# Optimization experiments

Hardware: AMD Instinct MI355X
Metric: run time of the kernel (lower is better)

## Reference

```python
import math
import jax, jax.numpy as jnp
import numpy as np

EMB = 768
HEADS = 12
HEAD_DIM = EMB // HEADS


def setup_inputs() -> dict:
    key = jax.random.key(0)
    k_x, k_wqkv, k_bqkv, k_wo, k_bo = jax.random.split(key, 5)
    B, N = 8, 1024
    lim_qkv = 1.0 / math.sqrt(EMB)
    lim_o = 1.0 / math.sqrt(EMB)
    return {
        "x": jax.random.normal(k_x, (B, N, EMB), dtype=jnp.float32),
        # torch nn.Linear convention: W has shape [out_features, in_features]
        "w_qkv": jax.random.uniform(k_wqkv, (3 * EMB, EMB), minval=-lim_qkv, maxval=lim_qkv, dtype=jnp.float32),
        "b_qkv": jax.random.uniform(k_bqkv, (3 * EMB,), minval=-lim_qkv, maxval=lim_qkv, dtype=jnp.float32),
        "w_out": jax.random.uniform(k_wo, (EMB, EMB), minval=-lim_o, maxval=lim_o, dtype=jnp.float32),
        "b_out": jax.random.uniform(k_bo, (EMB,), minval=-lim_o, maxval=lim_o, dtype=jnp.float32),
    }


def reference(x, w_qkv, b_qkv, w_out, b_out):
    B, N, _ = x.shape
    # fused QKV projection: [B, N, 3*EMB]
    qkv = jnp.einsum("bne,fe->bnf", x, w_qkv) + b_qkv
    qkv = qkv.reshape(B, N, 3, HEADS, HEAD_DIM)
    q, k, v = qkv[:, :, 0], qkv[:, :, 1], qkv[:, :, 2]  # [B, N, H, D]
    scale = 1.0 / math.sqrt(HEAD_DIM)
    # scores: [B, H, N, N]
    scores = jnp.einsum("bnhd,bmhd->bhnm", q, k) * scale
    attn = jax.nn.softmax(scores, axis=-1)
    # dropout is identity in eval mode (deterministic reference)
    out = jnp.einsum("bhnm,bmhd->bnhd", attn, v).reshape(B, N, EMB)
    out = jnp.einsum("bne,fe->bnf", out, w_out) + b_out
    return out, attn
```

## Files before the change

kernel.cpp:

```cpp
#include <hip/hip_runtime.h>
#include <hip/hip_bf16.h>
#include <cstddef>
#include <cstdint>

#define B_     8
#define N_     1024
#define EMB_   768
#define HEADS_ 12
#define HDIM_  64
#define M_TOK  (B_ * N_)
#define QKVF   (3 * EMB_)
#define OUT_ELEMS  ((size_t)M_TOK * EMB_)
#define ATTN_ELEMS ((size_t)B_ * HEADS_ * N_ * N_)

using short8  = __attribute__((ext_vector_type(8))) short;
using floatx4 = __attribute__((ext_vector_type(4))) float;

__device__ __forceinline__ short f32_to_bf16(float f) {
    union { float f; unsigned u; } x; x.f = f;
    unsigned r = x.u + 0x7FFFu + ((x.u >> 16) & 1u);
    return (short)(r >> 16);
}

__device__ __forceinline__ void gload_lds16(const void* g, void* l) {
    __builtin_amdgcn_global_load_lds(
        (const __attribute__((address_space(1))) void*)g,
        (__attribute__((address_space(3))) void*)l, 16, 0, 0);
}

__device__ __forceinline__ floatx4 mfma16(short8 a, short8 b, floatx4 c) {
    return __builtin_amdgcn_mfma_f32_16x16x32_bf16(a, b, c, 0, 0, 0);
}

__global__ __launch_bounds__(256) void cast_kernel(const float* __restrict__ in,
                                                   short* __restrict__ out) {
    const int i = (blockIdx.x * 256 + threadIdx.x) * 4;
    const float4 v = *reinterpret_cast<const float4*>(&in[i]);
    short s0 = f32_to_bf16(v.x), s1 = f32_to_bf16(v.y);
    short s2 = f32_to_bf16(v.z), s3 = f32_to_bf16(v.w);
    using short4v = __attribute__((ext_vector_type(4))) short;
    short4v s = {s0, s1, s2, s3};
    *reinterpret_cast<short4v*>(&out[i]) = s;
}

template <int OUT_BF16>
__global__ __launch_bounds__(256) void mfma_gemm_bt(
    const short* __restrict__ A, int lda,
    const short* __restrict__ Bm, int ldb,
    const float* __restrict__ bias,
    void* __restrict__ Cp, int ldc, int K)
{
    __shared__ short As[128 * 32];
    __shared__ short Bs[128 * 32];

    const int t = threadIdx.x, lane = t & 63, w = t >> 6;
    const int wy = w >> 1, wx = w & 1;
    const int row0 = blockIdx.y * 128;
    const int col0 = blockIdx.x * 128;
    const int m = lane & 15, kc = lane >> 4;
    const int sw = kc ^ ((m >> 1) & 3);

    floatx4 acc[4][4] = {};

    for (int k0 = 0; k0 < K; k0 += 32) {
        __syncthreads();
#pragma unroll
        for (int p = 0; p < 2; ++p) {
            const int ci = p * 256 + w * 64 + lane;
            const int r = ci >> 2, c = ci & 3;
            const int g = c ^ ((r >> 1) & 3);
            gload_lds16(&A[(size_t)(row0 + r) * lda + k0 + g * 8],
                        &As[(p * 256 + w * 64) * 8]);
            gload_lds16(&Bm[(size_t)(col0 + r) * ldb + k0 + g * 8],
                        &Bs[(p * 256 + w * 64) * 8]);
        }
        __syncthreads();

        short8 af[4], bf[4];
#pragma unroll
        for (int i = 0; i < 4; ++i)
            af[i] = *reinterpret_cast<const short8*>(
                &As[((wy * 64 + i * 16 + m) * 4 + sw) * 8]);
#pragma unroll
        for (int j = 0; j < 4; ++j)
            bf[j] = *reinterpret_cast<const short8*>(
                &Bs[((wx * 64 + j * 16 + m) * 4 + sw) * 8]);
#pragma unroll
        for (int i = 0; i < 4; ++i)
#pragma unroll
            for (int j = 0; j < 4; ++j)
                acc[i][j] = mfma16(af[i], bf[j], acc[i][j]);
    }

    const int rq = lane >> 4;
#pragma unroll
    for (int i = 0; i < 4; ++i) {
        const int rbase = row0 + wy * 64 + i * 16 + rq * 4;
#pragma unroll
        for (int j = 0; j < 4; ++j) {
            const int cc = col0 + wx * 64 + j * 16 + m;
            const float bb = bias[cc];
#pragma unroll
            for (int rg = 0; rg < 4; ++rg) {
                const float v = acc[i][j][rg] + bb;
                if (OUT_BF16)
                    ((short*)Cp)[(size_t)(rbase + rg) * ldc + cc] = f32_to_bf16(v);
                else
                    ((float*)Cp)[(size_t)(rbase + rg) * ldc + cc] = v;
            }
        }
    }
}

__global__ __launch_bounds__(256) void transpose_v(
    const short* __restrict__ qkv, short* __restrict__ Vt)
{
    __shared__ short T[64][72];
    const int bh = blockIdx.y, b = bh / HEADS_, h = bh % HEADS_;
    const int m0 = blockIdx.x * 64;
    const int t = threadIdx.x;
    const size_t vbase = (size_t)(b * N_) * QKVF + 2 * EMB_ + h * HDIM_;

#pragma unroll
    for (int p = 0; p < 2; ++p) {
        const int ci = p * 256 + t;
        const int r = ci >> 3, c = ci & 7;
        const short8 v = *reinterpret_cast<const short8*>(
            &qkv[vbase + (size_t)(m0 + r) * QKVF + c * 8]);
#pragma unroll
        for (int j = 0; j < 8; ++j) T[c * 8 + j][r] = v[j];
    }
    __syncthreads();
#pragma unroll
    for (int p = 0; p < 2; ++p) {
        const int ci = p * 256 + t;
        const int d = ci >> 3, c = ci & 7;
        short8 v;
#pragma unroll
        for (int j = 0; j < 8; ++j) v[j] = T[d][c * 8 + j];
        *reinterpret_cast<short8*>(&Vt[((size_t)bh * 64 + d) * N_ + m0 + c * 8]) = v;
    }
}

__global__ __launch_bounds__(256) void fused_attn(
    const short* __restrict__ qkv, const short* __restrict__ Vt,
    float* __restrict__ attn, short* __restrict__ O)
{
    __shared__ short Qs[128 * 64];
    __shared__ short Ks[2][64 * 64];
    __shared__ short Vs[2][64 * 64];
    __shared__ short Ps[128 * 72];
    __shared__ float rowM[128];
    __shared__ float rowS[128];

    const int t = threadIdx.x, lane = t & 63, w = t >> 6;
    const int bh = blockIdx.y, b = bh / HEADS_, h = bh % HEADS_;
    const int n0 = blockIdx.x * 128;
    const int m = lane & 15, kc = lane >> 4;
    const size_t qbase = (size_t)(b * N_) * QKVF + h * HDIM_;
    const size_t kbase = qbase + EMB_;

#define STAGE_K(buf, k0src)                                                   \
    do {                                                                      \
        _Pragma("unroll")                                                     \
        for (int p = 0; p < 2; ++p) {                                         \
            const int ci = p * 256 + w * 64 + lane;                           \
            const int r = ci >> 3, c = ci & 7;                                \
            const int g = c ^ (r & 7);                                        \
            gload_lds16(&qkv[kbase + (size_t)((k0src) + r) * QKVF + g * 8],   \
                        &Ks[buf][(p * 256 + w * 64) * 8]);                    \
        }                                                                     \
    } while (0)

#define STAGE_V(buf, k0src)                                                   \
    do {                                                                      \
        _Pragma("unroll")                                                     \
        for (int p = 0; p < 2; ++p) {                                         \
            const int ci = p * 256 + w * 64 + lane;                           \
            const int r = ci >> 3, c = ci & 7;                                \
            const int g = c ^ (r & 7);                                        \
            gload_lds16(&Vt[((size_t)bh * 64 + r) * N_ + (k0src) + g * 8],    \
                        &Vs[buf][(p * 256 + w * 64) * 8]);                    \
        }                                                                     \
    } while (0)

#pragma unroll
    for (int p = 0; p < 4; ++p) {
        const int ci = p * 256 + w * 64 + lane;
        const int r = ci >> 3, c = ci & 7;
        const int g = c ^ (r & 7);
        gload_lds16(&qkv[qbase + (size_t)(n0 + r) * QKVF + g * 8],
                    &Qs[(p * 256 + w * 64) * 8]);
    }
    STAGE_K(0, 0);
    __syncthreads();

    short8 qf[2][2];
#pragma unroll
    for (int i = 0; i < 2; ++i)
#pragma unroll
        for (int ks = 0; ks < 2; ++ks) {
            const int row = w * 32 + i * 16 + m;
            const int chunk = ks * 4 + kc;
            qf[i][ks] = *reinterpret_cast<const short8*>(
                &Qs[(row * 8 + (chunk ^ (m & 7))) * 8]);
        }

    float m_run[2][4], s_run[2][4];
#pragma unroll
    for (int i = 0; i < 2; ++i)
#pragma unroll
        for (int rg = 0; rg < 4; ++rg) { m_run[i][rg] = -1e30f; s_run[i][rg] = 0.0f; }

    for (int s = 0; s < 16; ++s) {
        const int cur = s & 1;
        if (s < 15) STAGE_K(cur ^ 1, (s + 1) * 64);

        floatx4 acc[2][4] = {};
#pragma unroll
        for (int ks = 0; ks < 2; ++ks) {
            const int chunk = ks * 4 + kc;
            const int pcs = chunk ^ (m & 7);
            short8 bfr[4];
#pragma unroll
            for (int j = 0; j < 4; ++j)
                bfr[j] = *reinterpret_cast<const short8*>(
                    &Ks[cur][((j * 16 + m) * 8 + pcs) * 8]);
#pragma unroll
            for (int i = 0; i < 2; ++i)
#pragma unroll
                for (int j = 0; j < 4; ++j)
                    acc[i][j] = mfma16(qf[i][ks], bfr[j], acc[i][j]);
        }

#pragma unroll
        for (int i = 0; i < 2; ++i)
#pragma unroll
            for (int rg = 0; rg < 4; ++rg) {
                const float x0 = acc[i][0][rg] * 0.125f;
                const float x1 = acc[i][1][rg] * 0.125f;
                const float x2 = acc[i][2][rg] * 0.125f;
                const float x3 = acc[i][3][rg] * 0.125f;
                float tm = fmaxf(fmaxf(x0, x1), fmaxf(x2, x3));
#pragma unroll
                for (int off = 1; off < 16; off <<= 1)
                    tm = fmaxf(tm, __shfl_xor(tm, off));
                const float mn = fmaxf(m_run[i][rg], tm);
                float ts = expf(x0 - mn) + expf(x1 - mn)
                         + expf(x2 - mn) + expf(x3 - mn);
#pragma unroll
                for (int off = 1; off < 16; off <<= 1)
                    ts += __shfl_xor(ts, off);
                s_run[i][rg] = s_run[i][rg] * expf(m_run[i][rg] - mn) + ts;
                m_run[i][rg] = mn;
            }
        __syncthreads();
    }

    if (m == 0) {
#pragma unroll
        for (int i = 0; i < 2; ++i)
#pragma unroll
            for (int rg = 0; rg < 4; ++rg) {
                const int row = w * 32 + i * 16 + kc * 4 + rg;
                rowM[row] = m_run[i][rg];
                rowS[row] = s_run[i][rg];
            }
    }
    STAGE_K(0, 0);
    STAGE_V(0, 0);
    __syncthreads();

    float Mreg[2][4], Sinv[2][4];
#pragma unroll
    for (int i = 0; i < 2; ++i)
#pragma unroll
        for (int rg = 0; rg < 4; ++rg) {
            const int row = w * 32 + i * 16 + kc * 4 + rg;
            Mreg[i][rg] = rowM[row];
            Sinv[i][rg] = 1.0f / rowS[row];
        }

    floatx4 accO[2][4] = {};

    for (int s = 0; s < 16; ++s) {
        const int cur = s & 1;
        if (s < 15) { STAGE_K(cur ^ 1, (s + 1) * 64); STAGE_V(cur ^ 1, (s + 1) * 64); }

        floatx4 acc[2][4] = {};
#pragma unroll
        for (int ks = 0; ks < 2; ++ks) {
            const int chunk = ks * 4 + kc;
            const int pcs = chunk ^ (m & 7);
            short8 bfr[4];
#pragma unroll
            for (int j = 0; j < 4; ++j)
                bfr[j] = *reinterpret_cast<const short8*>(
                    &Ks[cur][((j * 16 + m) * 8 + pcs) * 8]);
#pragma unroll
            for (int i = 0; i < 2; ++i)
#pragma unroll
                for (int j = 0; j < 4; ++j)
                    acc[i][j] = mfma16(qf[i][ks], bfr[j], acc[i][j]);
        }

        const int k0 = s * 64;
#pragma unroll
        for (int i = 0; i < 2; ++i)
#pragma unroll
            for (int rg = 0; rg < 4; ++rg) {
                const int row = w * 32 + i * 16 + kc * 4 + rg;
                const float M = Mreg[i][rg], inv = Sinv[i][rg];
                float* dst = &attn[((size_t)bh * N_ + n0 + row) * N_ + k0];
#pragma unroll
                for (int j = 0; j < 4; ++j) {
                    const float p = expf(acc[i][j][rg] * 0.125f - M) * inv;
                    __builtin_nontemporal_store(p, &dst[j * 16 + m]);
                    Ps[row * 72 + j * 16 + m] = f32_to_bf16(p);
                }
            }

#pragma unroll
        for (int ks = 0; ks < 2; ++ks) {
            const int chunk = ks * 4 + kc;
            const int pcs = chunk ^ (m & 7);
            short8 pa[2], vb[4];
#pragma unroll
            for (int i = 0; i < 2; ++i)
                pa[i] = *reinterpret_cast<const short8*>(
                    &Ps[(w * 32 + i * 16 + m) * 72 + chunk * 8]);
#pragma unroll
            for (int j = 0; j < 4; ++j)
                vb[j] = *reinterpret_cast<const short8*>(
                    &Vs[cur][((j * 16 + m) * 8 + pcs) * 8]);
#pragma unroll
            for (int i = 0; i < 2; ++i)
#pragma unroll
                for (int j = 0; j < 4; ++j)
                    accO[i][j] = mfma16(pa[i], vb[j], accO[i][j]);
        }
        __syncthreads();
    }

#pragma unroll
    for (int i = 0; i < 2; ++i)
#pragma unroll
        for (int j = 0; j < 4; ++j)
#pragma unroll
            for (int rg = 0; rg < 4; ++rg) {
                const int row = n0 + w * 32 + i * 16 + kc * 4 + rg;
                const int col = h * HDIM_ + j * 16 + m;
                O[(size_t)(b * N_ + row) * EMB_ + col] = f32_to_bf16(accO[i][j][rg]);
            }
#undef STAGE_K
#undef STAGE_V
}

extern "C" void kernel_launch(void* const* d_in, const int* in_sizes, int n_in,
                              void* d_out, int out_size, void* d_ws, size_t ws_size,
                              hipStream_t stream)
{
    const float* x     = (const float*)d_in[0];
    const float* w_qkv = (const float*)d_in[1];
    const float* b_qkv = (const float*)d_in[2];
    const float* w_out = (const float*)d_in[3];
    const float* b_out = (const float*)d_in[4];

    float* out  = (float*)d_out;
    float* attn = out + OUT_ELEMS;

    short* qkvb = (short*)d_ws;
    short* xb   = qkvb + (size_t)M_TOK * QKVF;
    short* wqb  = xb   + OUT_ELEMS;
    short* wob  = wqb  + (size_t)QKVF * EMB_;
    short* Vt   = wob  + (size_t)EMB_ * EMB_;
    short* O    = Vt   + (size_t)B_ * HEADS_ * HDIM_ * N_;

    const dim3 blk(256);

    cast_kernel<<<dim3(OUT_ELEMS / 1024), blk, 0, stream>>>(x, xb);
    cast_kernel<<<dim3((QKVF * EMB_) / 1024), blk, 0, stream>>>(w_qkv, wqb);
    cast_kernel<<<dim3((EMB_ * EMB_) / 1024), blk, 0, stream>>>(w_out, wob);

    mfma_gemm_bt<1><<<dim3(QKVF / 128, M_TOK / 128), blk, 0, stream>>>(
        xb, EMB_, wqb, EMB_, b_qkv, qkvb, QKVF, EMB_);

    transpose_v<<<dim3(N_ / 64, B_ * HEADS_), blk, 0, stream>>>(qkvb, Vt);

    fused_attn<<<dim3(N_ / 128, B_ * HEADS_), blk, 0, stream>>>(qkvb, Vt, attn, O);

    mfma_gemm_bt<0><<<dim3(EMB_ / 128, M_TOK / 128), blk, 0, stream>>>(
        O, EMB_, wob, EMB_, b_out, out, EMB_, EMB_);
}
```

Baseline: 695.0 us.

## Cut softmax shuffles, reuse Q buffer for P, switch to exp2 and swap grid

The first pass now keeps per-lane running max and sum and merges them across the 16 lanes once at the end, instead of shuffle-reducing on every tile. The exponentials use exp2f with the scale and log2(e) folded into one constant. The Q shared buffer is reused for P with an XOR swizzle, which removes the separate Ps, rowM and rowS arrays and lowers LDS use so occupancy can rise. The grid axes are swapped so neighbouring blocks work on different heads, and the attention store becomes a normal store instead of a nontemporal one, which may change how the large attn write uses the cache.

```diff
diff --git a/kernel.cpp b/kernel.cpp
--- a/kernel.cpp
+++ b/kernel.cpp
@@ -13,6 +13,8 @@
 #define OUT_ELEMS  ((size_t)M_TOK * EMB_)
 #define ATTN_ELEMS ((size_t)B_ * HEADS_ * N_ * N_)
 
+#define CEXP 0.18033688011112042f
+
 using short8  = __attribute__((ext_vector_type(8))) short;
 using floatx4 = __attribute__((ext_vector_type(4))) float;
 
@@ -146,16 +148,13 @@
     const short* __restrict__ qkv, const short* __restrict__ Vt,
     float* __restrict__ attn, short* __restrict__ O)
 {
-    __shared__ short Qs[128 * 64];
+    __shared__ short QP[128 * 64];
     __shared__ short Ks[2][64 * 64];
     __shared__ short Vs[2][64 * 64];
-    __shared__ short Ps[128 * 72];
-    __shared__ float rowM[128];
-    __shared__ float rowS[128];
 
     const int t = threadIdx.x, lane = t & 63, w = t >> 6;
-    const int bh = blockIdx.y, b = bh / HEADS_, h = bh % HEADS_;
-    const int n0 = blockIdx.x * 128;
+    const int bh = blockIdx.x, b = bh / HEADS_, h = bh % HEADS_;
+    const int n0 = blockIdx.y * 128;
     const int m = lane & 15, kc = lane >> 4;
     const size_t qbase = (size_t)(b * N_) * QKVF + h * HDIM_;
     const size_t kbase = qbase + EMB_;
@@ -190,7 +189,7 @@
         const int r = ci >> 3, c = ci & 7;
         const int g = c ^ (r & 7);
         gload_lds16(&qkv[qbase + (size_t)(n0 + r) * QKVF + g * 8],
-                    &Qs[(p * 256 + w * 64) * 8]);
+                    &QP[(p * 256 + w * 64) * 8]);
     }
     STAGE_K(0, 0);
     __syncthreads();
@@ -203,7 +202,7 @@
             const int row = w * 32 + i * 16 + m;
             const int chunk = ks * 4 + kc;
             qf[i][ks] = *reinterpret_cast<const short8*>(
-                &Qs[(row * 8 + (chunk ^ (m & 7))) * 8]);
+                &QP[(row * 8 + (chunk ^ (m & 7))) * 8]);
         }
 
     float m_run[2][4], s_run[2][4];
@@ -237,49 +236,40 @@
         for (int i = 0; i < 2; ++i)
 #pragma unroll
             for (int rg = 0; rg < 4; ++rg) {
-                const float x0 = acc[i][0][rg] * 0.125f;
-                const float x1 = acc[i][1][rg] * 0.125f;
-                const float x2 = acc[i][2][rg] * 0.125f;
-                const float x3 = acc[i][3][rg] * 0.125f;
-                float tm = fmaxf(fmaxf(x0, x1), fmaxf(x2, x3));
-#pragma unroll
-                for (int off = 1; off < 16; off <<= 1)
-                    tm = fmaxf(tm, __shfl_xor(tm, off));
-                const float mn = fmaxf(m_run[i][rg], tm);
-                float ts = expf(x0 - mn) + expf(x1 - mn)
-                         + expf(x2 - mn) + expf(x3 - mn);
-#pragma unroll
-                for (int off = 1; off < 16; off <<= 1)
-                    ts += __shfl_xor(ts, off);
-                s_run[i][rg] = s_run[i][rg] * expf(m_run[i][rg] - mn) + ts;
+                const float x0 = acc[i][0][rg], x1 = acc[i][1][rg];
+                const float x2 = acc[i][2][rg], x3 = acc[i][3][rg];
+                const float tm = fmaxf(fmaxf(x0, x1), fmaxf(x2, x3));
+                const float mo = m_run[i][rg];
+                const float mn = fmaxf(mo, tm);
+                const float f  = exp2f((mo - mn) * CEXP);
+                const float ts = exp2f((x0 - mn) * CEXP) + exp2f((x1 - mn) * CEXP)
+                               + exp2f((x2 - mn) * CEXP) + exp2f((x3 - mn) * CEXP);
+                s_run[i][rg] = s_run[i][rg] * f + ts;
                 m_run[i][rg] = mn;
             }
         __syncthreads();
     }
 
-    if (m == 0) {
-#pragma unroll
-        for (int i = 0; i < 2; ++i)
-#pragma unroll
-            for (int rg = 0; rg < 4; ++rg) {
-                const int row = w * 32 + i * 16 + kc * 4 + rg;
-                rowM[row] = m_run[i][rg];
-                rowS[row] = s_run[i][rg];
-            }
-    }
+    float Mreg[2][4], Sinv[2][4];
+#pragma unroll
+    for (int i = 0; i < 2; ++i)
+#pragma unroll
+        for (int rg = 0; rg < 4; ++rg) {
+            float M = m_run[i][rg];
+#pragma unroll
+            for (int off = 1; off < 16; off <<= 1)
+                M = fmaxf(M, __shfl_xor(M, off));
+            float sc = s_run[i][rg] * exp2f((m_run[i][rg] - M) * CEXP);
+#pragma unroll
+            for (int off = 1; off < 16; off <<= 1)
+                sc += __shfl_xor(sc, off);
+            Mreg[i][rg] = M;
+            Sinv[i][rg] = 1.0f / sc;
+        }
+
     STAGE_K(0, 0);
     STAGE_V(0, 0);
     __syncthreads();
-
-    float Mreg[2][4], Sinv[2][4];
-#pragma unroll
-    for (int i = 0; i < 2; ++i)
-#pragma unroll
-        for (int rg = 0; rg < 4; ++rg) {
-            const int row = w * 32 + i * 16 + kc * 4 + rg;
-            Mreg[i][rg] = rowM[row];
-            Sinv[i][rg] = 1.0f / rowS[row];
-        }
 
     floatx4 accO[2][4] = {};
 
@@ -311,12 +301,15 @@
             for (int rg = 0; rg < 4; ++rg) {
                 const int row = w * 32 + i * 16 + kc * 4 + rg;
                 const float M = Mreg[i][rg], inv = Sinv[i][rg];
+                const int r7 = row & 7;
                 float* dst = &attn[((size_t)bh * N_ + n0 + row) * N_ + k0];
 #pragma unroll
                 for (int j = 0; j < 4; ++j) {
-                    const float p = expf(acc[i][j][rg] * 0.125f - M) * inv;
-                    __builtin_nontemporal_store(p, &dst[j * 16 + m]);
-                    Ps[row * 72 + j * 16 + m] = f32_to_bf16(p);
+                    const float p = exp2f((acc[i][j][rg] - M) * CEXP) * inv;
+                    dst[j * 16 + m] = p;
+                    const int col = j * 16 + m;
+                    const int pc = (col >> 3) ^ r7;
+                    QP[row * 64 + pc * 8 + (col & 7)] = f32_to_bf16(p);
                 }
             }
 
@@ -326,9 +319,11 @@
             const int pcs = chunk ^ (m & 7);
             short8 pa[2], vb[4];
 #pragma unroll
-            for (int i = 0; i < 2; ++i)
+            for (int i = 0; i < 2; ++i) {
+                const int ra = w * 32 + i * 16 + m;
                 pa[i] = *reinterpret_cast<const short8*>(
-                    &Ps[(w * 32 + i * 16 + m) * 72 + chunk * 8]);
+                    &QP[(ra * 8 + pcs) * 8]);
+            }
 #pragma unroll
             for (int j = 0; j < 4; ++j)
                 vb[j] = *reinterpret_cast<const short8*>(
@@ -387,7 +382,7 @@
 
     transpose_v<<<dim3(N_ / 64, B_ * HEADS_), blk, 0, stream>>>(qkvb, Vt);
 
-    fused_attn<<<dim3(N_ / 128, B_ * HEADS_), blk, 0, stream>>>(qkvb, Vt, attn, O);
+    fused_attn<<<dim3(B_ * HEADS_, N_ / 128), blk, 0, stream>>>(qkvb, Vt, attn, O);
 
     mfma_gemm_bt<0><<<dim3(EMB_ / 128, M_TOK / 128), blk, 0, stream>>>(
         O, EMB_, wob, EMB_, b_out, out, EMB_, EMB_);
```

Result: faster. 617.0 us (-11.2%).
